# Kernel optimization log

Hardware: AMD Instinct MI355X
Metric: run time of the kernel (lower is better)

Reference implementation:

```python
import jax, jax.numpy as jnp
import numpy as np

T, N, C, L, H, NL = 32, 16, 64, 64, 128, 128
NA = 2 * L              # action logits come from the K gather -> 2*L slots
TOTAL = 3 + H + NA + L  # packed RecurrentState width: a,p,v,h,a_probs,p_probs


def _gru_cell(x, h, Wih, Whh, bih, bhh):
    # PyTorch GRUCell math
    gi = x @ Wih.T + bih
    gh = h @ Whh.T + bhh
    i_r, i_z, i_n = jnp.split(gi, 3, axis=-1)
    h_r, h_z, h_n = jnp.split(gh, 3, axis=-1)
    r = jax.nn.sigmoid(i_r + h_r)
    z = jax.nn.sigmoid(i_z + h_z)
    n = jnp.tanh(i_n + r * h_n)
    return (1.0 - z) * n + z * h


def _gru_seq(xs, Wih, Whh, bih, bhh):
    # xs: (steps, B, H) -> outputs (steps, B, H), zero initial state (torch default)
    h0 = jnp.zeros((xs.shape[1], Whh.shape[1]), xs.dtype)
    def step(h, x):
        hn = _gru_cell(x, h, Wih, Whh, bih, bhh)
        return hn, hn
    _, out = jax.lax.scan(step, h0, xs)
    return out


def _forward(cond, rnn_hxs, emb, aemb, tg_Wih_f, tg_Whh_f, tg_bih_f, tg_bhh_f, tg_Wih_b, tg_Whh_b, tg_bih_b, tg_bhh_b, gc_Wih, gc_Whh, gc_bih, gc_bhh, f_W0, f_b0, f_W1, f_b1, f_W2, f_b2, c_W0, c_b0, c_W1, c_b1, c_W2, c_b2, a_W0, a_b0, a_W1, a_b1, a_Wc, a_bc, lines_obs, given_a, given_p):
    relu = jax.nn.relu
    hx = rnn_hxs[0]                       # (N, TOTAL): a(1) p(1) v(1) h(H) a_probs(NA) p_probs(L)
    h0 = hx[:, 3:3 + H]
    a_init = hx[:, 0].astype(jnp.int32)   # A[-1] = hx.a (zeros at episode start)

    # --- bidirectional task encoder over all L cyclic rolls of line embeddings ---
    M = emb[lines_obs[0]]                 # (N, L, H); only t=0 lines are used
    gi = jnp.transpose(M, (1, 0, 2))      # (L, N, H)
    j = jnp.arange(L)
    idx = (j[None, :] - j[:, None]) % L   # rolled[i, j] = gi[(j - i) % L]  (torch.roll)
    rolled = gi[idx]                      # (L_roll, L, N, H)

    def bidir(xs):
        of = _gru_seq(xs, tg_Wih_f, tg_Whh_f, tg_bih_f, tg_bhh_f)
        ob = _gru_seq(xs[::-1], tg_Wih_b, tg_Whh_b, tg_bih_b, tg_bhh_b)[::-1]
        return jnp.concatenate([of, ob], axis=-1)

    S = jax.vmap(bidir)(rolled)           # (L, L, N, 2H)
    K = S.reshape(L, L, N, 2, H).transpose(2, 0, 1, 3, 4).reshape(N, L, 2 * L, H)

    # --- time-batched MLPs (independent of recurrent state) ---
    q_all = relu(relu(relu(cond @ f_W0 + f_b0) @ f_W1 + f_b1) @ f_W2 + f_b2)   # (T,N,H)
    all_inputs = jnp.concatenate([cond, lines_obs.astype(cond.dtype)], axis=-1)
    v_all = relu(relu(all_inputs @ c_W0 + c_b0) @ c_W1 + c_b1) @ c_W2 + c_b2   # (T,N,1)

    a_prev = jnp.concatenate([a_init[None], given_a[:-1]], axis=0)             # A[t-1] per step
    Rn = jnp.arange(N)

    def step(h, inp):
        ap, pt, qt = inp
        hn = _gru_cell(aemb[ap], h, gc_Wih, gc_Whh, gc_bih, gc_bhh)
        x = relu(hn @ a_W0 + a_b0)
        x = relu(x @ a_W1 + a_b1)
        p_probs = jax.nn.softmax(x @ a_Wc + a_bc, axis=-1)                     # (N, L)
        k = K[Rn, pt]                                                          # (N, 2L, H)
        a_probs = jax.nn.softmax(jnp.einsum('nkh,nh->nk', k, qt), axis=-1)     # (N, 2L)
        return hn, (a_probs, p_probs)

    _, (a_probs, p_probs) = jax.lax.scan(step, h0, (a_prev, given_p, q_all))

    # original yields hx.h (the INITIAL hidden) at every step -- faithful to source
    h_rep = jnp.broadcast_to(h0[None], (T, N, H))
    hx_out = jnp.concatenate([
        given_a.astype(cond.dtype)[..., None],
        given_p.astype(cond.dtype)[..., None],
        v_all, h_rep, a_probs, p_probs], axis=-1)                              # (T, N, TOTAL)
    return hx_out


def setup_inputs():
    ki = iter(jax.random.split(jax.random.key(0), 48))
    def nrm(shape, s):
        return jax.random.normal(next(ki), shape, jnp.float32) * s
    sH = float(1.0 / np.sqrt(H))
    inp = {}
    inp["cond"] = jax.random.normal(next(ki), (T, N, C), jnp.float32)
    inp["lines_obs"] = jax.random.randint(next(ki), (T, N, L), 0, NL, jnp.int32)
    inp["given_a"] = jax.random.randint(next(ki), (T, N), 0, NA, jnp.int32)
    inp["given_p"] = jax.random.randint(next(ki), (T, N), 0, L, jnp.int32)
    inp["rnn_hxs"] = jnp.zeros((1, N, TOTAL), jnp.float32)
    inp["emb"] = nrm((NL, H), 1.0)
    inp["aemb"] = nrm((NA, H), 1.0)
    for nm in ("tg_Wih_f", "tg_Whh_f", "tg_Wih_b", "tg_Whh_b", "gc_Wih", "gc_Whh"):
        inp[nm] = nrm((3 * H, H), sH)
    for nm in ("tg_bih_f", "tg_bhh_f", "tg_bih_b", "tg_bhh_b", "gc_bih", "gc_bhh"):
        inp[nm] = nrm((3 * H,), sH)
    inp["f_W0"] = nrm((C, H), float(1.0 / np.sqrt(C))); inp["f_b0"] = jnp.zeros((H,), jnp.float32)
    inp["f_W1"] = nrm((H, H), sH); inp["f_b1"] = jnp.zeros((H,), jnp.float32)
    inp["f_W2"] = nrm((H, H), sH); inp["f_b2"] = jnp.zeros((H,), jnp.float32)
    Din = C + L
    inp["c_W0"] = nrm((Din, H), float(1.0 / np.sqrt(Din))); inp["c_b0"] = jnp.zeros((H,), jnp.float32)
    inp["c_W1"] = nrm((H, H), sH); inp["c_b1"] = jnp.zeros((H,), jnp.float32)
    inp["c_W2"] = nrm((H, 1), sH); inp["c_b2"] = jnp.zeros((1,), jnp.float32)
    inp["a_W0"] = nrm((H, H), sH); inp["a_b0"] = jnp.zeros((H,), jnp.float32)
    inp["a_W1"] = nrm((H, H), sH); inp["a_b1"] = jnp.zeros((H,), jnp.float32)
    inp["a_Wc"] = nrm((H, L), sH); inp["a_bc"] = jnp.zeros((L,), jnp.float32)
    return inp


def reference(cond, lines_obs, given_a, given_p, rnn_hxs, emb, aemb, tg_Wih_f, tg_Whh_f, tg_bih_f, tg_bhh_f, tg_Wih_b, tg_Whh_b, tg_bih_b, tg_bhh_b, gc_Wih, gc_Whh, gc_bih, gc_bhh, f_W0, f_b0, f_W1, f_b1, f_W2, f_b2, c_W0, c_b0, c_W1, c_b1, c_W2, c_b2, a_W0, a_b0, a_W1, a_b1, a_Wc, a_bc):
    hx_out = _forward(cond, rnn_hxs, emb, aemb, tg_Wih_f, tg_Whh_f, tg_bih_f, tg_bhh_f, tg_Wih_b, tg_Whh_b, tg_bih_b, tg_bhh_b, gc_Wih, gc_Whh, gc_bih, gc_bhh, f_W0, f_b0, f_W1, f_b1, f_W2, f_b2, c_W0, c_b0, c_W1, c_b1, c_W2, c_b2, a_W0, a_b0, a_W1, a_b1, a_Wc, a_bc, lines_obs, given_a, given_p)
    return (hx_out, hx_out[-1:])
```

## Files before the change

kernel.cpp:

```cpp
#include <hip/hip_runtime.h>
#include <hip/hip_bf16.h>

#define T_ 32
#define N_ 16
#define C_ 64
#define L_ 64
#define H_ 128
#define G3 384
#define TOT 323

#define OFF_XF 0
#define OFF_XB 393216
#define OFF_XG 786432
#define OFF_Q  983040
#define OFF_V  1048576
#define OFF_HS 1049088
#define KM_OFF 4458496

typedef __attribute__((ext_vector_type(8))) short s16x8;
typedef __attribute__((ext_vector_type(4))) float fx4;

__device__ __forceinline__ unsigned short f2bf(float f) {
  unsigned u = __builtin_bit_cast(unsigned, f);
  unsigned r = (u + 0x7FFFu + ((u >> 16) & 1u)) >> 16;
  return (unsigned short)r;
}
__device__ __forceinline__ float bf2f(unsigned short u) {
  unsigned v = ((unsigned)u) << 16;
  return __builtin_bit_cast(float, v);
}
__device__ __forceinline__ float sigm(float x) {
  return __builtin_amdgcn_rcpf(1.f + __expf(-x));
}
__device__ __forceinline__ float tanh_(float x) {
  return 1.f - 2.f * __builtin_amdgcn_rcpf(__expf(2.f * x) + 1.f);
}

__global__ __launch_bounds__(384) void pre_kernel(
    const float* __restrict__ cond, const int* __restrict__ lines,
    const int* __restrict__ given_a, const float* __restrict__ hx,
    const float* __restrict__ emb, const float* __restrict__ aemb,
    const float* __restrict__ Wih_f, const float* __restrict__ bih_f,
    const float* __restrict__ Wih_b, const float* __restrict__ bih_b,
    const float* __restrict__ gc_Wih, const float* __restrict__ gc_bih,
    const float* __restrict__ f_W0, const float* __restrict__ f_b0,
    const float* __restrict__ f_W1, const float* __restrict__ f_b1,
    const float* __restrict__ f_W2, const float* __restrict__ f_b2,
    const float* __restrict__ c_W0, const float* __restrict__ c_b0,
    const float* __restrict__ c_W1, const float* __restrict__ c_b1,
    const float* __restrict__ c_W2, const float* __restrict__ c_b2,
    float* __restrict__ wsf)
{
  __shared__ __align__(16) float xs[2048];
  const int bid = blockIdx.x, tid = threadIdx.x;

  if (bid < 160) {
    const float* W;
    const float* bias;
    float* outp;
    if (bid < 128) {
      int l = bid >> 1, d = bid & 1;
      for (int idx = tid; idx < 2048; idx += 384) {
        int n = idx >> 7, k = idx & 127;
        int e = lines[n * L_ + l];
        xs[idx] = emb[e * H_ + k];
      }
      W = d ? Wih_b : Wih_f;
      bias = d ? bih_b : bih_f;
      outp = wsf + (d ? OFF_XB : OFF_XF) + l * (N_ * G3);
    } else {
      int t = bid - 128;
      for (int idx = tid; idx < 2048; idx += 384) {
        int n = idx >> 7, k = idx & 127;
        int ap = (t == 0) ? (int)hx[n * TOT] : given_a[(t - 1) * N_ + n];
        xs[idx] = aemb[ap * H_ + k];
      }
      W = gc_Wih; bias = gc_bih;
      outp = wsf + OFF_XG + t * (N_ * G3);
    }
    __syncthreads();
    const int c = tid;
    float acc[16];
    float b = bias[c];
    #pragma unroll
    for (int n = 0; n < 16; ++n) acc[n] = b;
    const float4* wr = (const float4*)(W + c * H_);
    #pragma unroll 4
    for (int k4 = 0; k4 < 32; ++k4) {
      float4 w = wr[k4];
      #pragma unroll
      for (int n = 0; n < 16; ++n) {
        float4 x = ((const float4*)(xs + n * H_))[k4];
        acc[n] += w.x * x.x + w.y * x.y + w.z * x.z + w.w * x.w;
      }
    }
    #pragma unroll
    for (int n = 0; n < 16; ++n) outp[n * G3 + c] = acc[n];
  } else {
    int tn = bid - 160;
    float* x0 = xs;
    float* x1 = xs + 256;
    float* x2 = xs + 512;
    const int c = tid;
    if (c < 64) x0[c] = cond[tn * C_ + c];
    __syncthreads();
    if (c < 128) {
      float s = f_b0[c];
      #pragma unroll 8
      for (int k = 0; k < 64; ++k) s += x0[k] * f_W0[k * H_ + c];
      x1[c] = fmaxf(s, 0.f);
    }
    __syncthreads();
    if (c < 128) {
      float s = f_b1[c];
      #pragma unroll 8
      for (int k = 0; k < 128; ++k) s += x1[k] * f_W1[k * H_ + c];
      x2[c] = fmaxf(s, 0.f);
    }
    __syncthreads();
    if (c < 128) {
      float s = f_b2[c];
      #pragma unroll 8
      for (int k = 0; k < 128; ++k) s += x2[k] * f_W2[k * H_ + c];
      wsf[OFF_Q + tn * H_ + c] = fmaxf(s, 0.f);
    }
    __syncthreads();
    if (c < 64) {
      x0[c] = cond[tn * C_ + c];
      x0[64 + c] = (float)lines[tn * L_ + c];
    }
    __syncthreads();
    if (c < 128) {
      float s = c_b0[c];
      #pragma unroll 8
      for (int k = 0; k < 128; ++k) s += x0[k] * c_W0[k * H_ + c];
      x1[c] = fmaxf(s, 0.f);
    }
    __syncthreads();
    if (c < 128) {
      float s = c_b1[c];
      #pragma unroll 8
      for (int k = 0; k < 128; ++k) s += x1[k] * c_W1[k * H_ + c];
      x2[c] = fmaxf(s, 0.f);
    }
    __syncthreads();
    if (c < 128) x0[c] = x2[c] * c_W2[c];
    __syncthreads();
    if (c == 0) {
      float s = c_b2[0];
      for (int k = 0; k < 128; ++k) s += x0[k];
      wsf[OFF_V + tn] = s;
    }
  }
}

__global__ __launch_bounds__(512) void mid_kernel(
    const float* __restrict__ Whh_f, const float* __restrict__ Whh_b,
    const float* __restrict__ bhh_f, const float* __restrict__ bhh_b,
    const float* __restrict__ gc_Whh, const float* __restrict__ gc_bhh,
    const float* __restrict__ hx,
    float* __restrict__ wsf, unsigned short* __restrict__ Km)
{
  __shared__ __align__(16) unsigned short hls[4096];
  const int bid = blockIdx.x, tid = threadIdx.x;

  if (bid < 128) {
    const int i = bid >> 1, d = bid & 1;
    const float* Whh = d ? Whh_b : Whh_f;
    const float* bhh = d ? bhh_b : bhh_f;
    const float* Xd = wsf + (d ? OFF_XB : OFF_XF);
    const int w = tid >> 6, lane = tid & 63;
    const int col16 = lane & 15, krow = lane >> 4;
    const int bq = krow * 4;
    const int cc = w * 16 + col16;

    for (int idx = tid; idx < 4096; idx += 512) hls[idx] = 0;

    s16x8 Bf[3][4];
    float bias[3];
    int colg[3];
    #pragma unroll
    for (int g = 0; g < 3; ++g) {
      int cg = (g * 8 + w) * 16 + col16;
      colg[g] = cg;
      bias[g] = bhh[cg];
      #pragma unroll
      for (int kb = 0; kb < 4; ++kb) {
        const float* src = Whh + cg * H_ + kb * 32 + krow * 8;
        float4 aa = *(const float4*)(src);
        float4 bb = *(const float4*)(src + 4);
        s16x8 s;
        s[0] = (short)f2bf(aa.x); s[1] = (short)f2bf(aa.y);
        s[2] = (short)f2bf(aa.z); s[3] = (short)f2bf(aa.w);
        s[4] = (short)f2bf(bb.x); s[5] = (short)f2bf(bb.y);
        s[6] = (short)f2bf(bb.z); s[7] = (short)f2bf(bb.w);
        Bf[g][kb] = s;
      }
    }
    float hreg[4] = {0.f, 0.f, 0.f, 0.f};
    char* lbase = (char*)hls;
    __syncthreads();

    float xpc[3][4];
    {
      int jj0 = d ? 63 : 0;
      int lx0 = (jj0 - i) & 63;
      #pragma unroll
      for (int g = 0; g < 3; ++g)
        #pragma unroll
        for (int r = 0; r < 4; ++r)
          xpc[g][r] = Xd[(lx0 * N_ + bq + r) * G3 + colg[g]];
    }

    int p = 0;
    #pragma unroll 1
    for (int s = 0; s < 64; ++s) {
      const int jj = d ? (63 - s) : s;
      const int jn = d ? ((62 - s) & 63) : ((s + 1) & 63);
      const int lxn = (jn - i) & 63;
      float xpn[3][4];
      #pragma unroll
      for (int g = 0; g < 3; ++g)
        #pragma unroll
        for (int r = 0; r < 4; ++r)
          xpn[g][r] = Xd[(lxn * N_ + bq + r) * G3 + colg[g]];
      s16x8 Af[4];
      {
        const int ra = col16;
        #pragma unroll
        for (int kb = 0; kb < 4; ++kb) {
          int ab = ((ra * 256 + kb * 64 + krow * 16) ^ ((ra & 7) << 4));
          Af[kb] = *(const s16x8*)(lbase + p * 4096 + ab);
        }
      }
      fx4 acc[3];
      #pragma unroll
      for (int g = 0; g < 3; ++g) {
        fx4 a;
        a[0] = bias[g]; a[1] = bias[g]; a[2] = bias[g]; a[3] = bias[g];
        #pragma unroll
        for (int kb = 0; kb < 4; ++kb)
          a = __builtin_amdgcn_mfma_f32_16x16x32_bf16(Af[kb], Bf[g][kb], a, 0, 0, 0);
        acc[g] = a;
      }
      char* wbb = lbase + (p ^ 1) * 4096;
      #pragma unroll
      for (int r = 0; r < 4; ++r) {
        int b = bq + r;
        float rr = sigm(xpc[0][r] + acc[0][r]);
        float zz = sigm(xpc[1][r] + acc[1][r]);
        float nn = tanh_(xpc[2][r] + rr * acc[2][r]);
        float hn = nn + zz * (hreg[r] - nn);
        hreg[r] = hn;
        unsigned short u = f2bf(hn);
        int wb = ((b * 256 + cc * 2) ^ ((b & 7) << 4));
        *(unsigned short*)(wbb + wb) = u;
        Km[((b * 64 + i) * 128 + (2 * jj + d)) * 128 + cc] = u;
      }
      asm volatile("s_waitcnt lgkmcnt(0)" ::: "memory");
      __builtin_amdgcn_s_barrier();
      asm volatile("" ::: "memory");
      p ^= 1;
      #pragma unroll
      for (int g = 0; g < 3; ++g)
        #pragma unroll
        for (int r = 0; r < 4; ++r)
          xpc[g][r] = xpn[g][r];
    }
  } else {
    const int n = bid - 128;
    float* hcur = (float*)hls;
    float* gh = ((float*)hls) + 128;
    float4 wreg[32];
    float bias_ = 0.f;
    if (tid < 384) {
      const float4* wr = (const float4*)(gc_Whh + tid * H_);
      #pragma unroll
      for (int k4 = 0; k4 < 32; ++k4) wreg[k4] = wr[k4];
      bias_ = gc_bhh[tid];
    }
    if (tid < 128) hcur[tid] = hx[n * TOT + 3 + tid];
    __syncthreads();
    #pragma unroll 1
    for (int t = 0; t < 32; ++t) {
      if (tid < 384) {
        float a0 = bias_, a1 = 0.f, a2 = 0.f, a3 = 0.f;
        const float4* hv = (const float4*)hcur;
        #pragma unroll
        for (int k4 = 0; k4 < 32; k4 += 4) {
          float4 w0 = wreg[k4],     h0 = hv[k4];
          float4 w1 = wreg[k4 + 1], h1 = hv[k4 + 1];
          float4 w2 = wreg[k4 + 2], h2 = hv[k4 + 2];
          float4 w3 = wreg[k4 + 3], h3 = hv[k4 + 3];
          a0 += w0.x * h0.x + w0.y * h0.y + w0.z * h0.z + w0.w * h0.w;
          a1 += w1.x * h1.x + w1.y * h1.y + w1.z * h1.z + w1.w * h1.w;
          a2 += w2.x * h2.x + w2.y * h2.y + w2.z * h2.z + w2.w * h2.w;
          a3 += w3.x * h3.x + w3.y * h3.y + w3.z * h3.z + w3.w * h3.w;
        }
        gh[tid] = (a0 + a1) + (a2 + a3);
      }
      __syncthreads();
      if (tid < 128) {
        const float* xgp = wsf + OFF_XG + (t * N_ + n) * G3;
        float rr = sigm(xgp[tid] + gh[tid]);
        float zz = sigm(xgp[128 + tid] + gh[128 + tid]);
        float nn = tanh_(xgp[256 + tid] + rr * gh[256 + tid]);
        float hn = nn + zz * (hcur[tid] - nn);
        hcur[tid] = hn;
        wsf[OFF_HS + (t * N_ + n) * H_ + tid] = hn;
      }
      __syncthreads();
    }
  }
}

__global__ __launch_bounds__(128) void post_kernel(
    const int* __restrict__ given_a, const int* __restrict__ given_p,
    const float* __restrict__ hx,
    const float* __restrict__ a_W0, const float* __restrict__ a_b0,
    const float* __restrict__ a_W1, const float* __restrict__ a_b1,
    const float* __restrict__ a_Wc, const float* __restrict__ a_bc,
    const float* __restrict__ wsf, const unsigned short* __restrict__ Km,
    float* __restrict__ out)
{
  __shared__ __align__(16) unsigned short ktile[16384];
  __shared__ float xa[128], xb2[128], qv[128], red[4];
  const int tn = blockIdx.x, t = tn >> 4, n = tn & 15;
  const int c = threadIdx.x;
  const int lane = c & 63, wid = c >> 6;

  {
    int pt = given_p[tn];
    const s16x8* src = (const s16x8*)(Km + (n * 64 + pt) * 16384);
    #pragma unroll
    for (int it = 0; it < 16; ++it) {
      int chunk = it * 128 + c;
      s16x8 v = src[chunk];
      int byte = chunk * 16;
      int row = byte >> 8;
      *(s16x8*)((char*)ktile + (byte ^ ((row & 7) << 4))) = v;
    }
  }
  xa[c] = wsf[OFF_HS + tn * H_ + c];
  qv[c] = wsf[OFF_Q + tn * H_ + c];
  __syncthreads();
  float s = a_b0[c];
  #pragma unroll 8
  for (int k = 0; k < 128; ++k) s += xa[k] * a_W0[k * H_ + c];
  xb2[c] = fmaxf(s, 0.f);
  __syncthreads();
  s = a_b1[c];
  #pragma unroll 8
  for (int k = 0; k < 128; ++k) s += xb2[k] * a_W1[k * H_ + c];
  float x2v = fmaxf(s, 0.f);
  __syncthreads();
  xa[c] = x2v;
  __syncthreads();
  float al = 0.f;
  #pragma unroll
  for (int k8 = 0; k8 < 16; ++k8) {
    int byte = c * 256 + k8 * 16;
    s16x8 kv = *(const s16x8*)((const char*)ktile + (byte ^ ((c & 7) << 4)));
    #pragma unroll
    for (int j = 0; j < 8; ++j)
      al += bf2f((unsigned short)kv[j]) * qv[k8 * 8 + j];
  }
  float pl = 0.f;
  if (wid == 0) {
    float s2 = a_bc[lane];
    #pragma unroll 8
    for (int k = 0; k < 128; ++k) s2 += xa[k] * a_Wc[k * 64 + lane];
    pl = s2;
  }
  float m = al;
  #pragma unroll
  for (int off = 32; off; off >>= 1) m = fmaxf(m, __shfl_xor(m, off));
  if (lane == 0) red[wid] = m;
  __syncthreads();
  m = fmaxf(red[0], red[1]);
  float e = __expf(al - m);
  float ssum = e;
  #pragma unroll
  for (int off = 32; off; off >>= 1) ssum += __shfl_xor(ssum, off);
  if (lane == 0) red[2 + wid] = ssum;
  __syncthreads();
  float ap = e * __builtin_amdgcn_rcpf(red[2] + red[3]);

  const int obase = tn * TOT;
  const bool tail = (t == 31);
  const int tbase = 512 * TOT + n * TOT;
  out[obase + 131 + c] = ap;
  if (tail) out[tbase + 131 + c] = ap;
  {
    float hv = hx[n * TOT + 3 + c];
    out[obase + 3 + c] = hv;
    if (tail) out[tbase + 3 + c] = hv;
  }
  if (wid == 0) {
    float pm = pl;
    #pragma unroll
    for (int off = 32; off; off >>= 1) pm = fmaxf(pm, __shfl_xor(pm, off));
    float pe = __expf(pl - pm);
    float ps = pe;
    #pragma unroll
    for (int off = 32; off; off >>= 1) ps += __shfl_xor(ps, off);
    float pp = pe * __builtin_amdgcn_rcpf(ps);
    out[obase + 259 + lane] = pp;
    if (tail) out[tbase + 259 + lane] = pp;
  }
  if (c == 0) {
    float u0 = (float)given_a[tn];
    float u1 = (float)given_p[tn];
    float u2 = wsf[OFF_V + tn];
    out[obase + 0] = u0; out[obase + 1] = u1; out[obase + 2] = u2;
    if (tail) { out[tbase + 0] = u0; out[tbase + 1] = u1; out[tbase + 2] = u2; }
  }
}

extern "C" void kernel_launch(void* const* d_in, const int* in_sizes, int n_in,
                              void* d_out, int out_size, void* d_ws, size_t ws_size,
                              hipStream_t stream) {
  const float* cond  = (const float*)d_in[0];
  const int*   lines = (const int*)d_in[1];
  const int*   ga    = (const int*)d_in[2];
  const int*   gp    = (const int*)d_in[3];
  const float* hx    = (const float*)d_in[4];
  const float* emb   = (const float*)d_in[5];
  const float* aemb  = (const float*)d_in[6];
  const float* Wih_f = (const float*)d_in[7];
  const float* Whh_f = (const float*)d_in[8];
  const float* Wih_b = (const float*)d_in[9];
  const float* Whh_b = (const float*)d_in[10];
  const float* gcWih = (const float*)d_in[11];
  const float* gcWhh = (const float*)d_in[12];
  const float* bih_f = (const float*)d_in[13];
  const float* bhh_f = (const float*)d_in[14];
  const float* bih_b = (const float*)d_in[15];
  const float* bhh_b = (const float*)d_in[16];
  const float* gcbih = (const float*)d_in[17];
  const float* gcbhh = (const float*)d_in[18];
  const float* f_W0 = (const float*)d_in[19]; const float* f_b0 = (const float*)d_in[20];
  const float* f_W1 = (const float*)d_in[21]; const float* f_b1 = (const float*)d_in[22];
  const float* f_W2 = (const float*)d_in[23]; const float* f_b2 = (const float*)d_in[24];
  const float* c_W0 = (const float*)d_in[25]; const float* c_b0 = (const float*)d_in[26];
  const float* c_W1 = (const float*)d_in[27]; const float* c_b1 = (const float*)d_in[28];
  const float* c_W2 = (const float*)d_in[29]; const float* c_b2 = (const float*)d_in[30];
  const float* a_W0 = (const float*)d_in[31]; const float* a_b0 = (const float*)d_in[32];
  const float* a_W1 = (const float*)d_in[33]; const float* a_b1 = (const float*)d_in[34];
  const float* a_Wc = (const float*)d_in[35]; const float* a_bc = (const float*)d_in[36];

  float* wsf = (float*)d_ws;
  unsigned short* Km = (unsigned short*)((char*)d_ws + KM_OFF);
  float* out = (float*)d_out;

  pre_kernel<<<672, 384, 0, stream>>>(cond, lines, ga, hx, emb, aemb,
      Wih_f, bih_f, Wih_b, bih_b, gcWih, gcbih,
      f_W0, f_b0, f_W1, f_b1, f_W2, f_b2,
      c_W0, c_b0, c_W1, c_b1, c_W2, c_b2, wsf);
  mid_kernel<<<144, 512, 0, stream>>>(Whh_f, Whh_b, bhh_f, bhh_b,
      gcWhh, gcbhh, hx, wsf, Km);
  post_kernel<<<512, 128, 0, stream>>>(ga, gp, hx,
      a_W0, a_b0, a_W1, a_b1, a_Wc, a_bc, wsf, Km, out);
}
```

Baseline: 233.8 us.

## Use MFMA for input projections, pack both GRU directions per block, batch MLPs

The input-projection GEMMs in pre_kernel now run on bf16 MFMA instead of scalar FP32 FMA, and their output layout is transposed to gate-major with the batch index inner, so the recurrent kernel can load each step's inputs as float4 vectors. mid_kernel now runs the forward and backward directions of each roll in one block (64 blocks instead of 128), with each wave handling two column tiles. It also unrolls the step loop by two to double-buffer the prefetched inputs and advances the Km store offsets incrementally. The small MLP blocks process four time/batch rows per block and finish the value head with a wave shuffle reduction. The changes cut grid sizes and per-step memory cost, but bf16 rounding of the input projections adds error, and fewer recurrent blocks means fewer CUs are busy.

```diff
diff --git a/kernel.cpp b/kernel.cpp
--- a/kernel.cpp
+++ b/kernel.cpp
@@ -18,6 +18,7 @@
 #define KM_OFF 4458496
 
 typedef __attribute__((ext_vector_type(8))) short s16x8;
+typedef __attribute__((ext_vector_type(4))) short s16x4;
 typedef __attribute__((ext_vector_type(4))) float fx4;
 
 __device__ __forceinline__ unsigned short f2bf(float f) {
@@ -36,7 +37,7 @@
   return 1.f - 2.f * __builtin_amdgcn_rcpf(__expf(2.f * x) + 1.f);
 }
 
-__global__ __launch_bounds__(384) void pre_kernel(
+__global__ __launch_bounds__(512) void pre_kernel(
     const float* __restrict__ cond, const int* __restrict__ lines,
     const int* __restrict__ given_a, const float* __restrict__ hx,
     const float* __restrict__ emb, const float* __restrict__ aemb,
@@ -55,74 +56,109 @@
   const int bid = blockIdx.x, tid = threadIdx.x;
 
   if (bid < 160) {
-    const float* W;
-    const float* bias;
-    float* outp;
+    unsigned short* xbf = (unsigned short*)xs;
+    const float* W; const float* bias; float* outp;
+    {
+      int n = tid >> 5, k4 = (tid & 31) * 4;
+      const float* src;
+      if (bid < 128) {
+        int l = bid >> 1;
+        int e = lines[n * L_ + l];
+        src = emb + e * H_ + k4;
+      } else {
+        int t = bid - 128;
+        int ap = (t == 0) ? (int)hx[n * TOT] : given_a[(t - 1) * N_ + n];
+        src = aemb + ap * H_ + k4;
+      }
+      float4 v = *(const float4*)src;
+      s16x4 pk;
+      pk[0] = (short)f2bf(v.x); pk[1] = (short)f2bf(v.y);
+      pk[2] = (short)f2bf(v.z); pk[3] = (short)f2bf(v.w);
+      int byte = (n * 256 + k4 * 2) ^ ((n & 7) << 4);
+      *(s16x4*)((char*)xbf + byte) = pk;
+    }
     if (bid < 128) {
-      int l = bid >> 1, d = bid & 1;
-      for (int idx = tid; idx < 2048; idx += 384) {
-        int n = idx >> 7, k = idx & 127;
-        int e = lines[n * L_ + l];
-        xs[idx] = emb[e * H_ + k];
-      }
-      W = d ? Wih_b : Wih_f;
-      bias = d ? bih_b : bih_f;
-      outp = wsf + (d ? OFF_XB : OFF_XF) + l * (N_ * G3);
+      int d = bid & 1, l = bid >> 1;
+      W = d ? Wih_b : Wih_f;  bias = d ? bih_b : bih_f;
+      outp = wsf + (d ? OFF_XB : OFF_XF) + l * (G3 * N_);
     } else {
-      int t = bid - 128;
-      for (int idx = tid; idx < 2048; idx += 384) {
-        int n = idx >> 7, k = idx & 127;
-        int ap = (t == 0) ? (int)hx[n * TOT] : given_a[(t - 1) * N_ + n];
-        xs[idx] = aemb[ap * H_ + k];
-      }
       W = gc_Wih; bias = gc_bih;
-      outp = wsf + OFF_XG + t * (N_ * G3);
-    }
-    __syncthreads();
-    const int c = tid;
-    float acc[16];
-    float b = bias[c];
-    #pragma unroll
-    for (int n = 0; n < 16; ++n) acc[n] = b;
-    const float4* wr = (const float4*)(W + c * H_);
-    #pragma unroll 4
-    for (int k4 = 0; k4 < 32; ++k4) {
-      float4 w = wr[k4];
-      #pragma unroll
-      for (int n = 0; n < 16; ++n) {
-        float4 x = ((const float4*)(xs + n * H_))[k4];
-        acc[n] += w.x * x.x + w.y * x.y + w.z * x.z + w.w * x.w;
-      }
-    }
-    #pragma unroll
-    for (int n = 0; n < 16; ++n) outp[n * G3 + c] = acc[n];
+      outp = wsf + OFF_XG + (bid - 128) * (G3 * N_);
+    }
+    __syncthreads();
+    const int w = tid >> 6, lane = tid & 63;
+    const int col16 = lane & 15, krow = lane >> 4, bq = krow * 4;
+    s16x8 Af[4];
+    #pragma unroll
+    for (int kb = 0; kb < 4; ++kb) {
+      int ab = (col16 * 256 + kb * 64 + krow * 16) ^ ((col16 & 7) << 4);
+      Af[kb] = *(const s16x8*)((const char*)xbf + ab);
+    }
+    #pragma unroll
+    for (int g = 0; g < 3; ++g) {
+      int cg = (g * 8 + w) * 16 + col16;
+      float bv = bias[cg];
+      fx4 a; a[0] = bv; a[1] = bv; a[2] = bv; a[3] = bv;
+      #pragma unroll
+      for (int kb = 0; kb < 4; ++kb) {
+        const float* src = W + cg * H_ + kb * 32 + krow * 8;
+        float4 aa = *(const float4*)src;
+        float4 bb = *(const float4*)(src + 4);
+        s16x8 sv;
+        sv[0] = (short)f2bf(aa.x); sv[1] = (short)f2bf(aa.y);
+        sv[2] = (short)f2bf(aa.z); sv[3] = (short)f2bf(aa.w);
+        sv[4] = (short)f2bf(bb.x); sv[5] = (short)f2bf(bb.y);
+        sv[6] = (short)f2bf(bb.z); sv[7] = (short)f2bf(bb.w);
+        a = __builtin_amdgcn_mfma_f32_16x16x32_bf16(Af[kb], sv, a, 0, 0, 0);
+      }
+      #pragma unroll
+      for (int r = 0; r < 4; ++r)
+        outp[cg * 16 + bq + r] = a[r];
+    }
   } else {
-    int tn = bid - 160;
-    float* x0 = xs;
-    float* x1 = xs + 256;
-    float* x2 = xs + 512;
-    const int c = tid;
+    const int grp = tid >> 7, c = tid & 127;
+    const int tn = (bid - 160) * 4 + grp;
+    const int lane = c & 63, widg = c >> 6;
+    float* x0 = xs + grp * 384;
+    float* x1 = x0 + 128;
+    float* x2 = x0 + 256;
+    float* xred = xs + 1536;
     if (c < 64) x0[c] = cond[tn * C_ + c];
     __syncthreads();
-    if (c < 128) {
-      float s = f_b0[c];
-      #pragma unroll 8
-      for (int k = 0; k < 64; ++k) s += x0[k] * f_W0[k * H_ + c];
-      x1[c] = fmaxf(s, 0.f);
-    }
-    __syncthreads();
-    if (c < 128) {
-      float s = f_b1[c];
-      #pragma unroll 8
-      for (int k = 0; k < 128; ++k) s += x1[k] * f_W1[k * H_ + c];
-      x2[c] = fmaxf(s, 0.f);
-    }
-    __syncthreads();
-    if (c < 128) {
-      float s = f_b2[c];
-      #pragma unroll 8
-      for (int k = 0; k < 128; ++k) s += x2[k] * f_W2[k * H_ + c];
-      wsf[OFF_Q + tn * H_ + c] = fmaxf(s, 0.f);
+    {
+      float a0 = f_b0[c], a1 = 0.f, a2 = 0.f, a3 = 0.f;
+      #pragma unroll 4
+      for (int k = 0; k < 64; k += 4) {
+        a0 += x0[k] * f_W0[k * H_ + c];
+        a1 += x0[k + 1] * f_W0[(k + 1) * H_ + c];
+        a2 += x0[k + 2] * f_W0[(k + 2) * H_ + c];
+        a3 += x0[k + 3] * f_W0[(k + 3) * H_ + c];
+      }
+      x1[c] = fmaxf((a0 + a1) + (a2 + a3), 0.f);
+    }
+    __syncthreads();
+    {
+      float a0 = f_b1[c], a1 = 0.f, a2 = 0.f, a3 = 0.f;
+      #pragma unroll 4
+      for (int k = 0; k < 128; k += 4) {
+        a0 += x1[k] * f_W1[k * H_ + c];
+        a1 += x1[k + 1] * f_W1[(k + 1) * H_ + c];
+        a2 += x1[k + 2] * f_W1[(k + 2) * H_ + c];
+        a3 += x1[k + 3] * f_W1[(k + 3) * H_ + c];
+      }
+      x2[c] = fmaxf((a0 + a1) + (a2 + a3), 0.f);
+    }
+    __syncthreads();
+    {
+      float a0 = f_b2[c], a1 = 0.f, a2 = 0.f, a3 = 0.f;
+      #pragma unroll 4
+      for (int k = 0; k < 128; k += 4) {
+        a0 += x2[k] * f_W2[k * H_ + c];
+        a1 += x2[k + 1] * f_W2[(k + 1) * H_ + c];
+        a2 += x2[k + 2] * f_W2[(k + 2) * H_ + c];
+        a3 += x2[k + 3] * f_W2[(k + 3) * H_ + c];
+      }
+      wsf[OFF_Q + tn * H_ + c] = fmaxf((a0 + a1) + (a2 + a3), 0.f);
     }
     __syncthreads();
     if (c < 64) {
@@ -130,27 +166,39 @@
       x0[64 + c] = (float)lines[tn * L_ + c];
     }
     __syncthreads();
-    if (c < 128) {
-      float s = c_b0[c];
-      #pragma unroll 8
-      for (int k = 0; k < 128; ++k) s += x0[k] * c_W0[k * H_ + c];
-      x1[c] = fmaxf(s, 0.f);
-    }
-    __syncthreads();
-    if (c < 128) {
-      float s = c_b1[c];
-      #pragma unroll 8
-      for (int k = 0; k < 128; ++k) s += x1[k] * c_W1[k * H_ + c];
-      x2[c] = fmaxf(s, 0.f);
-    }
-    __syncthreads();
-    if (c < 128) x0[c] = x2[c] * c_W2[c];
-    __syncthreads();
-    if (c == 0) {
-      float s = c_b2[0];
-      for (int k = 0; k < 128; ++k) s += x0[k];
-      wsf[OFF_V + tn] = s;
-    }
+    {
+      float a0 = c_b0[c], a1 = 0.f, a2 = 0.f, a3 = 0.f;
+      #pragma unroll 4
+      for (int k = 0; k < 128; k += 4) {
+        a0 += x0[k] * c_W0[k * H_ + c];
+        a1 += x0[k + 1] * c_W0[(k + 1) * H_ + c];
+        a2 += x0[k + 2] * c_W0[(k + 2) * H_ + c];
+        a3 += x0[k + 3] * c_W0[(k + 3) * H_ + c];
+      }
+      x1[c] = fmaxf((a0 + a1) + (a2 + a3), 0.f);
+    }
+    __syncthreads();
+    {
+      float a0 = c_b1[c], a1 = 0.f, a2 = 0.f, a3 = 0.f;
+      #pragma unroll 4
+      for (int k = 0; k < 128; k += 4) {
+        a0 += x1[k] * c_W1[k * H_ + c];
+        a1 += x1[k + 1] * c_W1[(k + 1) * H_ + c];
+        a2 += x1[k + 2] * c_W1[(k + 2) * H_ + c];
+        a3 += x1[k + 3] * c_W1[(k + 3) * H_ + c];
+      }
+      x2[c] = fmaxf((a0 + a1) + (a2 + a3), 0.f);
+    }
+    __syncthreads();
+    {
+      float pv = x2[c] * c_W2[c];
+      #pragma unroll
+      for (int off = 32; off; off >>= 1) pv += __shfl_xor(pv, off);
+      if (lane == 0) xred[grp * 2 + widg] = pv;
+    }
+    __syncthreads();
+    if (c == 0)
+      wsf[OFF_V + tn] = c_b2[0] + xred[grp * 2] + xred[grp * 2 + 1];
   }
 }
 
@@ -161,114 +209,135 @@
     const float* __restrict__ hx,
     float* __restrict__ wsf, unsigned short* __restrict__ Km)
 {
-  __shared__ __align__(16) unsigned short hls[4096];
+  __shared__ __align__(16) unsigned short hls[8192];
   const int bid = blockIdx.x, tid = threadIdx.x;
 
-  if (bid < 128) {
-    const int i = bid >> 1, d = bid & 1;
+  if (bid < 64) {
+    const int i = bid;
+    const int wv = tid >> 6, lane = tid & 63;
+    const int d = wv >> 2, ws4 = wv & 3;
+    const int col16 = lane & 15, krow = lane >> 4, bq = krow * 4;
     const float* Whh = d ? Whh_b : Whh_f;
     const float* bhh = d ? bhh_b : bhh_f;
     const float* Xd = wsf + (d ? OFF_XB : OFF_XF);
-    const int w = tid >> 6, lane = tid & 63;
-    const int col16 = lane & 15, krow = lane >> 4;
-    const int bq = krow * 4;
-    const int cc = w * 16 + col16;
-
-    for (int idx = tid; idx < 4096; idx += 512) hls[idx] = 0;
-
-    s16x8 Bf[3][4];
-    float bias[3];
-    int colg[3];
-    #pragma unroll
-    for (int g = 0; g < 3; ++g) {
-      int cg = (g * 8 + w) * 16 + col16;
-      colg[g] = cg;
-      bias[g] = bhh[cg];
+
+    for (int idx = tid; idx < 8192; idx += 512) hls[idx] = 0;
+
+    s16x8 Bf[3][2][4];
+    float bias[3][2];
+    int voff[3][2];
+    #pragma unroll
+    for (int g = 0; g < 3; ++g)
+      #pragma unroll
+      for (int tl = 0; tl < 2; ++tl) {
+        int cg = g * 128 + ws4 * 32 + tl * 16 + col16;
+        bias[g][tl] = bhh[cg];
+        voff[g][tl] = cg * 16 + bq;
+        #pragma unroll
+        for (int kb = 0; kb < 4; ++kb) {
+          const float* src = Whh + cg * H_ + kb * 32 + krow * 8;
+          float4 aa = *(const float4*)src;
+          float4 bb = *(const float4*)(src + 4);
+          s16x8 sv;
+          sv[0] = (short)f2bf(aa.x); sv[1] = (short)f2bf(aa.y);
+          sv[2] = (short)f2bf(aa.z); sv[3] = (short)f2bf(aa.w);
+          sv[4] = (short)f2bf(bb.x); sv[5] = (short)f2bf(bb.y);
+          sv[6] = (short)f2bf(bb.z); sv[7] = (short)f2bf(bb.w);
+          Bf[g][tl][kb] = sv;
+        }
+      }
+    const int cc0 = ws4 * 32 + col16;
+    const int jj0 = d ? 63 : 0;
+    int koff[2][4];
+    #pragma unroll
+    for (int tl = 0; tl < 2; ++tl)
+      #pragma unroll
+      for (int r = 0; r < 4; ++r) {
+        int b = bq + r, cc = cc0 + tl * 16;
+        koff[tl][r] = (((b * 64 + i) * 128 + (2 * jj0 + d)) * 128 + cc) * 2;
+      }
+    const int kdel = d ? -512 : 512;
+    float hreg[2][4] = {{0.f, 0.f, 0.f, 0.f}, {0.f, 0.f, 0.f, 0.f}};
+    char* lb = (char*)hls + d * 8192;
+    int lx = (jj0 - i) & 63;
+    __syncthreads();
+
+    fx4 xpA[3][2], xpB[3][2];
+    {
+      const float* Xc = Xd + lx * (G3 * N_);
+      #pragma unroll
+      for (int g = 0; g < 3; ++g)
+        #pragma unroll
+        for (int tl = 0; tl < 2; ++tl)
+          xpA[g][tl] = *(const fx4*)(Xc + voff[g][tl]);
+    }
+
+    auto STEP = [&](int p, fx4 (&XC)[3][2], fx4 (&XN)[3][2]) {
+      s16x8 Af[4];
       #pragma unroll
       for (int kb = 0; kb < 4; ++kb) {
-        const float* src = Whh + cg * H_ + kb * 32 + krow * 8;
-        float4 aa = *(const float4*)(src);
-        float4 bb = *(const float4*)(src + 4);
-        s16x8 s;
-        s[0] = (short)f2bf(aa.x); s[1] = (short)f2bf(aa.y);
-        s[2] = (short)f2bf(aa.z); s[3] = (short)f2bf(aa.w);
-        s[4] = (short)f2bf(bb.x); s[5] = (short)f2bf(bb.y);
-        s[6] = (short)f2bf(bb.z); s[7] = (short)f2bf(bb.w);
-        Bf[g][kb] = s;
-      }
-    }
-    float hreg[4] = {0.f, 0.f, 0.f, 0.f};
-    char* lbase = (char*)hls;
-    __syncthreads();
-
-    float xpc[3][4];
-    {
-      int jj0 = d ? 63 : 0;
-      int lx0 = (jj0 - i) & 63;
+        int ab = (col16 * 256 + kb * 64 + krow * 16) ^ ((col16 & 7) << 4);
+        Af[kb] = *(const s16x8*)(lb + p * 4096 + ab);
+      }
+      int lxn = (d ? (lx - 1) : (lx + 1)) & 63;
+      {
+        const float* Xn = Xd + lxn * (G3 * N_);
+        #pragma unroll
+        for (int g = 0; g < 3; ++g)
+          #pragma unroll
+          for (int tl = 0; tl < 2; ++tl)
+            XN[g][tl] = *(const fx4*)(Xn + voff[g][tl]);
+      }
+      fx4 acc[3][2];
       #pragma unroll
       for (int g = 0; g < 3; ++g)
         #pragma unroll
-        for (int r = 0; r < 4; ++r)
-          xpc[g][r] = Xd[(lx0 * N_ + bq + r) * G3 + colg[g]];
-    }
-
-    int p = 0;
-    #pragma unroll 1
-    for (int s = 0; s < 64; ++s) {
-      const int jj = d ? (63 - s) : s;
-      const int jn = d ? ((62 - s) & 63) : ((s + 1) & 63);
-      const int lxn = (jn - i) & 63;
-      float xpn[3][4];
-      #pragma unroll
-      for (int g = 0; g < 3; ++g)
-        #pragma unroll
-        for (int r = 0; r < 4; ++r)
-          xpn[g][r] = Xd[(lxn * N_ + bq + r) * G3 + colg[g]];
-      s16x8 Af[4];
-      {
-        const int ra = col16;
-        #pragma unroll
-        for (int kb = 0; kb < 4; ++kb) {
-          int ab = ((ra * 256 + kb * 64 + krow * 16) ^ ((ra & 7) << 4));
-          Af[kb] = *(const s16x8*)(lbase + p * 4096 + ab);
+        for (int tl = 0; tl < 2; ++tl) {
+          float bv = bias[g][tl];
+          fx4 a; a[0] = bv; a[1] = bv; a[2] = bv; a[3] = bv;
+          #pragma unroll
+          for (int kb = 0; kb < 4; ++kb)
+            a = __builtin_amdgcn_mfma_f32_16x16x32_bf16(Af[kb], Bf[g][tl][kb], a, 0, 0, 0);
+          acc[g][tl] = a;
         }
-      }
-      fx4 acc[3];
-      #pragma unroll
-      for (int g = 0; g < 3; ++g) {
-        fx4 a;
-        a[0] = bias[g]; a[1] = bias[g]; a[2] = bias[g]; a[3] = bias[g];
-        #pragma unroll
-        for (int kb = 0; kb < 4; ++kb)
-          a = __builtin_amdgcn_mfma_f32_16x16x32_bf16(Af[kb], Bf[g][kb], a, 0, 0, 0);
-        acc[g] = a;
-      }
-      char* wbb = lbase + (p ^ 1) * 4096;
-      #pragma unroll
-      for (int r = 0; r < 4; ++r) {
-        int b = bq + r;
-        float rr = sigm(xpc[0][r] + acc[0][r]);
-        float zz = sigm(xpc[1][r] + acc[1][r]);
-        float nn = tanh_(xpc[2][r] + rr * acc[2][r]);
-        float hn = nn + zz * (hreg[r] - nn);
-        hreg[r] = hn;
-        unsigned short u = f2bf(hn);
-        int wb = ((b * 256 + cc * 2) ^ ((b & 7) << 4));
-        *(unsigned short*)(wbb + wb) = u;
-        Km[((b * 64 + i) * 128 + (2 * jj + d)) * 128 + cc] = u;
-      }
+      char* wb = lb + (p ^ 1) * 4096;
+      unsigned short uu[2][4];
+      #pragma unroll
+      for (int tl = 0; tl < 2; ++tl) {
+        int ccb = (cc0 + tl * 16) * 2;
+        #pragma unroll
+        for (int r = 0; r < 4; ++r) {
+          int b = bq + r;
+          float rr = sigm(XC[0][tl][r] + acc[0][tl][r]);
+          float zz = sigm(XC[1][tl][r] + acc[1][tl][r]);
+          float nn = tanh_(XC[2][tl][r] + rr * acc[2][tl][r]);
+          float hn = nn + zz * (hreg[tl][r] - nn);
+          hreg[tl][r] = hn;
+          unsigned short u = f2bf(hn);
+          uu[tl][r] = u;
+          *(unsigned short*)(wb + ((b * 256 + ccb) ^ ((b & 7) << 4))) = u;
+        }
+      }
+      #pragma unroll
+      for (int tl = 0; tl < 2; ++tl)
+        #pragma unroll
+        for (int r = 0; r < 4; ++r) {
+          *(unsigned short*)((char*)Km + koff[tl][r]) = uu[tl][r];
+          koff[tl][r] += kdel;
+        }
       asm volatile("s_waitcnt lgkmcnt(0)" ::: "memory");
       __builtin_amdgcn_s_barrier();
       asm volatile("" ::: "memory");
-      p ^= 1;
-      #pragma unroll
-      for (int g = 0; g < 3; ++g)
-        #pragma unroll
-        for (int r = 0; r < 4; ++r)
-          xpc[g][r] = xpn[g][r];
+      lx = lxn;
+    };
+
+    #pragma unroll 1
+    for (int it = 0; it < 32; ++it) {
+      STEP(0, xpA, xpB);
+      STEP(1, xpB, xpA);
     }
   } else {
-    const int n = bid - 128;
+    const int n = bid - 64;
     float* hcur = (float*)hls;
     float* gh = ((float*)hls) + 128;
     float4 wreg[32];
@@ -301,10 +370,10 @@
       }
       __syncthreads();
       if (tid < 128) {
-        const float* xgp = wsf + OFF_XG + (t * N_ + n) * G3;
-        float rr = sigm(xgp[tid] + gh[tid]);
-        float zz = sigm(xgp[128 + tid] + gh[128 + tid]);
-        float nn = tanh_(xgp[256 + tid] + rr * gh[256 + tid]);
+        const float* xgt = wsf + OFF_XG + t * (G3 * N_);
+        float rr = sigm(xgt[tid * 16 + n] + gh[tid]);
+        float zz = sigm(xgt[(128 + tid) * 16 + n] + gh[128 + tid]);
+        float nn = tanh_(xgt[(256 + tid) * 16 + n] + rr * gh[256 + tid]);
         float hn = nn + zz * (hcur[tid] - nn);
         hcur[tid] = hn;
         wsf[OFF_HS + (t * N_ + n) * H_ + tid] = hn;
@@ -453,11 +522,11 @@
   unsigned short* Km = (unsigned short*)((char*)d_ws + KM_OFF);
   float* out = (float*)d_out;
 
-  pre_kernel<<<672, 384, 0, stream>>>(cond, lines, ga, hx, emb, aemb,
+  pre_kernel<<<288, 512, 0, stream>>>(cond, lines, ga, hx, emb, aemb,
       Wih_f, bih_f, Wih_b, bih_b, gcWih, gcbih,
       f_W0, f_b0, f_W1, f_b1, f_W2, f_b2,
       c_W0, c_b0, c_W1, c_b1, c_W2, c_b2, wsf);
-  mid_kernel<<<144, 512, 0, stream>>>(Whh_f, Whh_b, bhh_f, bhh_b,
+  mid_kernel<<<80, 512, 0, stream>>>(Whh_f, Whh_b, bhh_f, bhh_b,
       gcWhh, gcbhh, hx, wsf, Km);
   post_kernel<<<512, 128, 0, stream>>>(ga, gp, hx,
       a_W0, a_b0, a_W1, a_b1, a_Wc, a_bc, wsf, Km, out);
```

New measurement: 257.0 us. 1.1x slower.
